# Kernel optimization log

Hardware: AMD Instinct MI355X
Metric: run time of the kernel (lower is better)

The kernel has to match this reference:

```python
import jax, jax.numpy as jnp
import numpy as np

# args of SimilarityLoss
B, N_WAY, N_SHOT, QUERY, NUM_SLOT, H = 128, 5, 1, 15, 32, 256
LAMBDA = 1.0


def setup_inputs() -> dict:
    key = jax.random.key(0)
    k1, k2, k3, k4 = jax.random.split(key, 4)
    out_f = jax.random.normal(k1, (B * N_WAY * (N_SHOT + QUERY), NUM_SLOT, H), jnp.float32)
    labels_support = jax.random.randint(k2, (B, N_WAY * N_SHOT), 0, N_WAY)  # unused by forward
    labels_query = jax.random.randint(k3, (B, QUERY, N_WAY, 1), 0, N_WAY)
    att_loss = jax.random.uniform(k4, (), jnp.float32)
    return {"out_f": out_f, "labels_support": labels_support,
            "labels_query": labels_query, "att_loss": att_loss, "mode": 0}


def _max_select(scores):
    # scores: [b, n_way, num_slot]. Greedy unique top-1 slot per class, classes in order.
    b, n_way, num_slot = scores.shape
    order = jnp.argsort(-scores, axis=-1)  # descending sort indices per class row
    used = jnp.zeros((b, num_slot), dtype=bool)
    rows = jnp.arange(b)
    sel = []
    for j in range(n_way):  # tiny fixed loop over classes (sequential dependency)
        row = order[:, j, :]                       # [b, num_slot]
        avail = ~used[rows[:, None], row]          # [b, num_slot]
        pos = jnp.argmax(avail, axis=1)            # first unused slot position
        pick = row[rows, pos]                      # [b]
        used = used.at[rows, pick].set(True)
        sel.append(pick)
    return jnp.stack(sel, axis=1)                  # [b, n_way]


def _normalize(x):
    # F.normalize(p=2, eps=1e-12) semantics
    n = jnp.linalg.norm(x, axis=-1, keepdims=True)
    return x / jnp.maximum(n, 1e-12)


def _forward(out_f, labels_query, att_loss):
    b = labels_query.shape[0]
    ns = b * N_WAY * N_SHOT
    sup = out_f[:ns].reshape(b, N_WAY, N_SHOT, NUM_SLOT, H).mean(axis=2)   # [b, n_way, num_slot, H]
    qry = out_f[ns:].reshape(b, N_WAY, QUERY, NUM_SLOT, H)

    sel = _max_select(sup.mean(-1))                                        # [b, n_way]

    idx_s = jnp.broadcast_to(sel[:, None, :, None], (b, N_WAY, N_WAY, H))
    sup_sel = jnp.take_along_axis(sup, idx_s, axis=2)                      # [b, n_way, n_way, H]
    idx_q = jnp.broadcast_to(sel[:, None, None, :, None], (b, N_WAY, QUERY, N_WAY, H))
    qry_sel = jnp.take_along_axis(qry, idx_q, axis=3).reshape(b, N_WAY * QUERY, N_WAY, H)

    sn = _normalize(sup_sel)
    qn = _normalize(qry_sel)

    diag = jnp.arange(N_WAY)
    proto = sn[:, diag, diag, :]                                           # support[i, j, j] -> [b, n_way, H]
    diff = jnp.sum((qn - proto[:, None, :, :]) ** 2, axis=-1)              # [b, n_way*query, n_way]

    # NB: raw-memory reshape (n_way, query) -> (query, n_way) exactly as the torch code does
    logits = jax.nn.log_softmax(-diff, axis=2).reshape(b, QUERY, N_WAY, N_WAY)

    nll = -jnp.take_along_axis(logits, labels_query, axis=3)               # [b, query, n_way, 1]
    loss = nll.mean() + jnp.float32(LAMBDA) * att_loss

    y_hat = jnp.argmax(logits, axis=3)                                     # [b, query, n_way]
    acc = jnp.mean((y_hat == labels_query[..., 0]).astype(jnp.float32))
    return loss, acc


def reference(out_f, labels_support, labels_query, att_loss, mode):
    return _forward(out_f, labels_query, att_loss)
```

## Files before the change

### kernel.cpp

```cpp
#include <hip/hip_runtime.h>

#define B_       128
#define N_WAY    5
#define QUERY    15
#define NUM_SLOT 32
#define H_       256
#define NS       (B_ * N_WAY)
#define NQ       (B_ * N_WAY * QUERY)
#define ROW      (NUM_SLOT * H_)
#define SPB      (N_WAY * QUERY)
#define RPB      (N_WAY * NUM_SLOT)
#define NBLK     (2 * B_)

__device__ __forceinline__ float wave_reduce(float v) {
    for (int m = 32; m > 0; m >>= 1) v += __shfl_xor(v, m, 64);
    return v;
}

__global__ __launch_bounds__(1024)
void k_fused(const float* __restrict__ out_f, const int* __restrict__ labels_q,
             float2* __restrict__ part) {
    int blk = blockIdx.x, b = blk >> 1, half = blk & 1;
    int t = threadIdx.x, wid = t >> 6, lane = t & 63;

    __shared__ float sc[RPB];
    __shared__ int ssel[N_WAY];
    __shared__ __align__(16) float pl[N_WAY][H_];
    __shared__ float p2s[N_WAY];
    __shared__ float s_n[16], s_c[16];

    const float* base = out_f + (size_t)b * RPB * H_;
    for (int i = wid; i < RPB; i += 32) {
        float4 v0 = ((const float4*)(base + (size_t)i * H_))[lane];
        float4 v1 = ((const float4*)(base + (size_t)(i + 16) * H_))[lane];
        float s0 = wave_reduce(v0.x + v0.y + v0.z + v0.w);
        float s1 = wave_reduce(v1.x + v1.y + v1.z + v1.w);
        if (lane == 0) { sc[i] = s0 * (1.0f / H_); sc[i + 16] = s1 * (1.0f / H_); }
    }
    __syncthreads();

    if (t == 0) {
        unsigned used = 0u;
        for (int j = 0; j < N_WAY; ++j) {
            float best = -INFINITY; int bi = 0;
            #pragma unroll
            for (int s = 0; s < NUM_SLOT; ++s) {
                bool ok = !((used >> s) & 1u);
                float v = sc[j * NUM_SLOT + s];
                if (ok && v > best) { best = v; bi = s; }
            }
            used |= 1u << bi;
            ssel[j] = bi;
        }
    }
    __syncthreads();

    if (wid < N_WAY) {
        int k = wid;
        float4 v = ((const float4*)(base + ((size_t)k * NUM_SLOT + ssel[k]) * H_))[lane];
        float s2 = wave_reduce(v.x*v.x + v.y*v.y + v.z*v.z + v.w*v.w);
        float inv = 1.0f / fmaxf(sqrtf(s2), 1e-12f);
        float4 nv = make_float4(v.x*inv, v.y*inv, v.z*inv, v.w*inv);
        *(float4*)&pl[k][lane * 4] = nv;
        float p2 = wave_reduce(nv.x*nv.x + nv.y*nv.y + nv.z*nv.z + nv.w*nv.w);
        if (lane == 0) p2s[k] = p2;
    }
    __syncthreads();

    int sBeg = half ? 38 : 0;
    int sEnd = half ? SPB : 38;
    float accn = 0.0f, accc = 0.0f;
    for (int s = sBeg + wid; s < sEnd; s += 16) {
        int id = b * SPB + s;
        const float* qrow = out_f + (size_t)(NS + id) * ROW;
        float4 qv[N_WAY];
        #pragma unroll
        for (int k = 0; k < N_WAY; ++k)
            qv[k] = ((const float4*)(qrow + (size_t)ssel[k] * H_))[lane];
        float diffs[N_WAY];
        #pragma unroll
        for (int k = 0; k < N_WAY; ++k) {
            float4 pv = *(const float4*)&pl[k][lane * 4];
            float s2 = qv[k].x*qv[k].x + qv[k].y*qv[k].y + qv[k].z*qv[k].z + qv[k].w*qv[k].w;
            float dt = qv[k].x*pv.x + qv[k].y*pv.y + qv[k].z*pv.z + qv[k].w*pv.w;
            for (int m = 32; m > 0; m >>= 1) {
                s2 += __shfl_xor(s2, m, 64);
                dt += __shfl_xor(dt, m, 64);
            }
            float inv = 1.0f / fmaxf(sqrtf(s2), 1e-12f);
            diffs[k] = s2 * inv * inv - 2.0f * dt * inv + p2s[k];
        }
        if (lane == 0) {
            int l = labels_q[id];
            float mn = diffs[0]; int am = 0;
            #pragma unroll
            for (int k = 1; k < N_WAY; ++k)
                if (diffs[k] < mn) { mn = diffs[k]; am = k; }
            float se = 0.0f;
            #pragma unroll
            for (int k = 0; k < N_WAY; ++k) se += expf(mn - diffs[k]);
            accn += diffs[l] - mn + logf(se);
            accc += (am == l) ? 1.0f : 0.0f;
        }
    }
    if (lane == 0) { s_n[wid] = accn; s_c[wid] = accc; }
    __syncthreads();

    if (t == 0) {
        float a = 0.0f, c = 0.0f;
        #pragma unroll
        for (int i = 0; i < 16; ++i) { a += s_n[i]; c += s_c[i]; }
        part[blk] = make_float2(a, c);
    }
}

__global__ __launch_bounds__(256)
void k_finalize(const float2* __restrict__ part, const float* __restrict__ att_loss,
                float* __restrict__ out) {
    __shared__ float sa[4], sb[4];
    int t = threadIdx.x, wid = t >> 6, lane = t & 63;
    float2 p = part[t];
    float a = wave_reduce(p.x);
    float c = wave_reduce(p.y);
    if (lane == 0) { sa[wid] = a; sb[wid] = c; }
    __syncthreads();
    if (t == 0) {
        float sn_ = sa[0] + sa[1] + sa[2] + sa[3];
        float sc_ = sb[0] + sb[1] + sb[2] + sb[3];
        out[0] = sn_ * (1.0f / NQ) + att_loss[0];
        out[1] = sc_ * (1.0f / NQ);
    }
}

extern "C" void kernel_launch(void* const* d_in, const int* in_sizes, int n_in,
                              void* d_out, int out_size, void* d_ws, size_t ws_size,
                              hipStream_t stream) {
    const float* out_f    = (const float*)d_in[0];
    const int*   labels_q = (const int*)d_in[2];
    const float* att_loss = (const float*)d_in[3];
    float* out = (float*)d_out;

    float2* part = (float2*)d_ws;

    k_fused   <<<NBLK, 1024, 0, stream>>>(out_f, labels_q, part);
    k_finalize<<<1,    256,  0, stream>>>(part, att_loss, out);
}
```

Measured before the change: 30.08 us.

## Fuse finalize into main kernel via flag handshake and wave-parallel slot selection

Drops the separate finalize launch. Each block now publishes its partial (loss, correct) pair atomically and raises a per-block flag, and block 0 spins until every flag is set before doing the final reduction and writing the outputs. The greedy unique-slot selection moves from a single-thread serial scan to a 64-lane shuffle argmax with ties broken toward the lower index. Flags are never cleared, so on repeated calls block 0 may see stale flags and read partials before they are rewritten. The spin-wait also relies on all 256 blocks being resident at the same time.

```diff
diff --git a/kernel.cpp b/kernel.cpp
--- a/kernel.cpp
+++ b/kernel.cpp
@@ -11,6 +11,10 @@
 #define SPB      (N_WAY * QUERY)
 #define RPB      (N_WAY * NUM_SLOT)
 #define NBLK     (2 * B_)
+#define TAG      0x13572468u
+
+typedef unsigned long long ull;
+union PU { ull u; float2 f; };
 
 __device__ __forceinline__ float wave_reduce(float v) {
     for (int m = 32; m > 0; m >>= 1) v += __shfl_xor(v, m, 64);
@@ -18,8 +22,9 @@
 }
 
 __global__ __launch_bounds__(1024)
-void k_fused(const float* __restrict__ out_f, const int* __restrict__ labels_q,
-             float2* __restrict__ part) {
+void k_all(const float* __restrict__ out_f, const int* __restrict__ labels_q,
+           const float* __restrict__ att_loss, ull* __restrict__ part,
+           unsigned* __restrict__ flags, float* __restrict__ out) {
     int blk = blockIdx.x, b = blk >> 1, half = blk & 1;
     int t = threadIdx.x, wid = t >> 6, lane = t & 63;
 
@@ -28,6 +33,7 @@
     __shared__ __align__(16) float pl[N_WAY][H_];
     __shared__ float p2s[N_WAY];
     __shared__ float s_n[16], s_c[16];
+    __shared__ float ra[4], rc[4];
 
     const float* base = out_f + (size_t)b * RPB * H_;
     for (int i = wid; i < RPB; i += 32) {
@@ -39,18 +45,19 @@
     }
     __syncthreads();
 
-    if (t == 0) {
+    if (t < 64) {
         unsigned used = 0u;
         for (int j = 0; j < N_WAY; ++j) {
-            float best = -INFINITY; int bi = 0;
-            #pragma unroll
-            for (int s = 0; s < NUM_SLOT; ++s) {
-                bool ok = !((used >> s) & 1u);
-                float v = sc[j * NUM_SLOT + s];
-                if (ok && v > best) { best = v; bi = s; }
+            float v = (lane < NUM_SLOT && !((used >> lane) & 1u))
+                        ? sc[j * NUM_SLOT + lane] : -INFINITY;
+            int idx = (lane < NUM_SLOT) ? lane : 63;
+            for (int m = 32; m > 0; m >>= 1) {
+                float v2 = __shfl_xor(v, m, 64);
+                int  i2 = __shfl_xor(idx, m, 64);
+                if (v2 > v || (v2 == v && i2 < idx)) { v = v2; idx = i2; }
             }
-            used |= 1u << bi;
-            ssel[j] = bi;
+            used |= 1u << idx;
+            if (lane == 0) ssel[j] = idx;
         }
     }
     __syncthreads();
@@ -110,25 +117,32 @@
         float a = 0.0f, c = 0.0f;
         #pragma unroll
         for (int i = 0; i < 16; ++i) { a += s_n[i]; c += s_c[i]; }
-        part[blk] = make_float2(a, c);
+        PU u; u.f = make_float2(a, c);
+        atomicExch(&part[blk], u.u);
+        __threadfence();
+        atomicExch(&flags[blk], TAG);
     }
-}
 
-__global__ __launch_bounds__(256)
-void k_finalize(const float2* __restrict__ part, const float* __restrict__ att_loss,
-                float* __restrict__ out) {
-    __shared__ float sa[4], sb[4];
-    int t = threadIdx.x, wid = t >> 6, lane = t & 63;
-    float2 p = part[t];
-    float a = wave_reduce(p.x);
-    float c = wave_reduce(p.y);
-    if (lane == 0) { sa[wid] = a; sb[wid] = c; }
-    __syncthreads();
-    if (t == 0) {
-        float sn_ = sa[0] + sa[1] + sa[2] + sa[3];
-        float sc_ = sb[0] + sb[1] + sb[2] + sb[3];
-        out[0] = sn_ * (1.0f / NQ) + att_loss[0];
-        out[1] = sc_ * (1.0f / NQ);
+    if (blk == 0) {
+        if (t < NBLK) {
+            while (atomicAdd(&flags[t], 0u) != TAG) __builtin_amdgcn_s_sleep(8);
+        }
+        __syncthreads();
+        __threadfence();
+        float a = 0.0f, c = 0.0f;
+        if (t < NBLK) {
+            PU u; u.u = atomicAdd(&part[t], 0ull);
+            a = wave_reduce(u.f.x);
+            c = wave_reduce(u.f.y);
+            if (lane == 0) { ra[wid] = a; rc[wid] = c; }
+        }
+        __syncthreads();
+        if (t == 0) {
+            float sn_ = ra[0] + ra[1] + ra[2] + ra[3];
+            float sc_ = rc[0] + rc[1] + rc[2] + rc[3];
+            out[0] = sn_ * (1.0f / NQ) + att_loss[0];
+            out[1] = sc_ * (1.0f / NQ);
+        }
     }
 }
 
@@ -140,8 +154,8 @@
     const float* att_loss = (const float*)d_in[3];
     float* out = (float*)d_out;
 
-    float2* part = (float2*)d_ws;
+    ull*      part  = (ull*)d_ws;
+    unsigned* flags = (unsigned*)(part + NBLK);
 
-    k_fused   <<<NBLK, 1024, 0, stream>>>(out_f, labels_q, part);
-    k_finalize<<<1,    256,  0, stream>>>(part, att_loss, out);
+    k_all<<<NBLK, 1024, 0, stream>>>(out_f, labels_q, att_loss, part, flags, out);
 }
```

Result: slower. 32.50 us (+8.1%).

## Split support slot-mean scoring into separate kernel and parallelize greedy select

Applied to the files above, without the earlier changes.

Moves the per-slot mean computation over support rows out of the fused kernel into a new k_scores kernel. It spreads 80 rows per block over 256 blocks instead of having both halves of each batch item redo all 160 rows. The greedy slot selection now runs as a wave-wide argmax with shuffles instead of a serial single-thread loop. This removes duplicated support reads and the serial critical path. In exchange it adds an extra kernel launch and a global round trip for the scores.

```diff
diff --git a/kernel.cpp b/kernel.cpp
--- a/kernel.cpp
+++ b/kernel.cpp
@@ -10,6 +10,7 @@
 #define ROW      (NUM_SLOT * H_)
 #define SPB      (N_WAY * QUERY)
 #define RPB      (N_WAY * NUM_SLOT)
+#define NROWS    (NS * NUM_SLOT)
 #define NBLK     (2 * B_)
 
 __device__ __forceinline__ float wave_reduce(float v) {
@@ -18,8 +19,29 @@
 }
 
 __global__ __launch_bounds__(1024)
-void k_fused(const float* __restrict__ out_f, const int* __restrict__ labels_q,
-             float2* __restrict__ part) {
+void k_scores(const float* __restrict__ out_f, float* __restrict__ scores_g) {
+    int t = threadIdx.x, wid = t >> 6, lane = t & 63;
+    const float* base = out_f + (size_t)blockIdx.x * 80 * H_;
+    float* og = scores_g + (size_t)blockIdx.x * 80;
+    #pragma unroll
+    for (int i = wid; i + 16 < 80; i += 32) {
+        float4 v0 = ((const float4*)(base + (size_t)i * H_))[lane];
+        float4 v1 = ((const float4*)(base + (size_t)(i + 16) * H_))[lane];
+        float s0 = wave_reduce(v0.x + v0.y + v0.z + v0.w);
+        float s1 = wave_reduce(v1.x + v1.y + v1.z + v1.w);
+        if (lane == 0) { og[i] = s0 * (1.0f / H_); og[i + 16] = s1 * (1.0f / H_); }
+    }
+    {
+        int i = wid + 64;
+        float4 v = ((const float4*)(base + (size_t)i * H_))[lane];
+        float s = wave_reduce(v.x + v.y + v.z + v.w);
+        if (lane == 0) og[i] = s * (1.0f / H_);
+    }
+}
+
+__global__ __launch_bounds__(1024)
+void k_fused(const float* __restrict__ out_f, const float* __restrict__ scores_g,
+             const int* __restrict__ labels_q, float2* __restrict__ part) {
     int blk = blockIdx.x, b = blk >> 1, half = blk & 1;
     int t = threadIdx.x, wid = t >> 6, lane = t & 63;
 
@@ -29,32 +51,27 @@
     __shared__ float p2s[N_WAY];
     __shared__ float s_n[16], s_c[16];
 
-    const float* base = out_f + (size_t)b * RPB * H_;
-    for (int i = wid; i < RPB; i += 32) {
-        float4 v0 = ((const float4*)(base + (size_t)i * H_))[lane];
-        float4 v1 = ((const float4*)(base + (size_t)(i + 16) * H_))[lane];
-        float s0 = wave_reduce(v0.x + v0.y + v0.z + v0.w);
-        float s1 = wave_reduce(v1.x + v1.y + v1.z + v1.w);
-        if (lane == 0) { sc[i] = s0 * (1.0f / H_); sc[i + 16] = s1 * (1.0f / H_); }
-    }
+    if (t < RPB) sc[t] = scores_g[(size_t)b * RPB + t];
     __syncthreads();
 
-    if (t == 0) {
+    if (t < 64) {
         unsigned used = 0u;
         for (int j = 0; j < N_WAY; ++j) {
-            float best = -INFINITY; int bi = 0;
-            #pragma unroll
-            for (int s = 0; s < NUM_SLOT; ++s) {
-                bool ok = !((used >> s) & 1u);
-                float v = sc[j * NUM_SLOT + s];
-                if (ok && v > best) { best = v; bi = s; }
+            float v = (lane < NUM_SLOT && !((used >> lane) & 1u))
+                        ? sc[j * NUM_SLOT + lane] : -INFINITY;
+            int idx = (lane < NUM_SLOT) ? lane : 63;
+            for (int m = 32; m > 0; m >>= 1) {
+                float v2 = __shfl_xor(v, m, 64);
+                int  i2 = __shfl_xor(idx, m, 64);
+                if (v2 > v || (v2 == v && i2 < idx)) { v = v2; idx = i2; }
             }
-            used |= 1u << bi;
-            ssel[j] = bi;
+            used |= 1u << idx;
+            if (lane == 0) ssel[j] = idx;
         }
     }
     __syncthreads();
 
+    const float* base = out_f + (size_t)b * RPB * H_;
     if (wid < N_WAY) {
         int k = wid;
         float4 v = ((const float4*)(base + ((size_t)k * NUM_SLOT + ssel[k]) * H_))[lane];
@@ -140,8 +157,10 @@
     const float* att_loss = (const float*)d_in[3];
     float* out = (float*)d_out;
 
-    float2* part = (float2*)d_ws;
+    float*  scores_g = (float*)d_ws;
+    float2* part     = (float2*)(scores_g + NROWS);
 
-    k_fused   <<<NBLK, 1024, 0, stream>>>(out_f, labels_q, part);
-    k_finalize<<<1,    256,  0, stream>>>(part, att_loss, out);
+    k_scores  <<<NROWS / 80, 1024, 0, stream>>>(out_f, scores_g);
+    k_fused   <<<NBLK,       1024, 0, stream>>>(out_f, scores_g, labels_q, part);
+    k_finalize<<<1,          256,  0, stream>>>(part, att_loss, out);
 }
```

New measurement: 28.50 us, median of 2. 1.06x faster.
